# Optimization experiments

Measured on AMD Instinct MI355X. Metric: run time of the kernel, lower is better.

Reference implementation:

```python
import jax, jax.numpy as jnp
import numpy as np

N_NODES = 50000
N_EDGES = 800000
C_FEAT = 96
HID = 96
C_CONST = 0.005


def _psi(v):
    return jnp.sign(v) * jnp.log(jnp.abs(v) + 1.0)


def setup_inputs() -> dict:
    key = jax.random.key(0)
    ks = jax.random.split(key, 16)
    d_e_in = 2 * C_FEAT + 2
    d_h_in = 2 * C_FEAT
    def w(k, fan_in, fan_out):
        return jax.random.normal(k, (fan_in, fan_out), jnp.float32) * (1.0 / np.sqrt(fan_in))
    return {
        "x": jax.random.normal(ks[0], (N_NODES, 4), jnp.float32),
        "h": jax.random.normal(ks[1], (N_NODES, C_FEAT), jnp.float32),
        "edge_i": jax.random.randint(ks[2], (N_EDGES,), 0, N_NODES, jnp.int32),
        "edge_j": jax.random.randint(ks[3], (N_EDGES,), 0, N_NODES, jnp.int32),
        "We1": w(ks[4], d_e_in, HID), "be1": jnp.zeros((HID,), jnp.float32),
        "We2": w(ks[5], HID, HID), "be2": jnp.zeros((HID,), jnp.float32),
        "Wm": w(ks[6], HID, 1), "bm": jnp.zeros((1,), jnp.float32),
        "Wh1": w(ks[7], d_h_in, HID), "bh1": jnp.zeros((HID,), jnp.float32),
        "Wh2": w(ks[8], HID, C_FEAT), "bh2": jnp.zeros((C_FEAT,), jnp.float32),
        "Wx1": w(ks[9], HID, HID), "bx1": jnp.zeros((HID,), jnp.float32),
        "Wx2": w(ks[10], HID, 1),  # bias-free last phi_x layer
    }


def reference(x, h, edge_i, edge_j, We1, be1, We2, be2, Wm, bm,
              Wh1, bh1, Wh2, bh2, Wx1, bx1, Wx2):
    n = x.shape[0]
    x_i = x[edge_i]            # (K,4)
    x_j = x[edge_j]            # (K,4)
    # Minkowski invariants: 2*t-component - full Euclidean sum == (+,-,-,-)
    d2 = jnp.square(x_i - x_j)
    norms = 2.0 * d2[..., 0] - jnp.sum(d2, axis=-1)
    z = x_i * x_j
    prods = 2.0 * z[..., 0] - jnp.sum(z, axis=-1)
    norms = _psi(norms)[:, None]   # (K,1)
    prods = _psi(prods)[:, None]   # (K,1)

    e_in = jnp.concatenate([h[edge_i], h[edge_j], norms, prods], axis=-1)  # (K,2C+2)
    m = jax.nn.relu(jax.nn.relu(e_in @ We1 + be1) @ We2 + be2)             # (K,HID)
    w_gate = jax.nn.sigmoid(m @ Wm + bm)                                   # (K,1)

    wm = jax.ops.segment_sum(w_gate * m, edge_i, num_segments=n)          # (N,HID)
    dh = jax.nn.relu(jnp.concatenate([h, wm], axis=-1) @ Wh1 + bh1) @ Wh2 + bh2
    h_out = h + dh

    phi_x = jax.nn.relu(m @ Wx1 + bx1) @ Wx2                              # (K,1)
    vals = phi_x * x_j                                                     # (K,4)
    s = jax.ops.segment_sum(vals, edge_i, num_segments=n)                 # (N,4)
    cnt = jax.ops.segment_sum(jnp.ones((vals.shape[0],), vals.dtype), edge_i, num_segments=n)
    mean = jnp.where(cnt[:, None] > 0, s / jnp.maximum(cnt[:, None], 1.0), 0.0)
    x_out = x + C_CONST * mean
    return (h_out, x_out)
```

## Files before the change

### kernel.cpp

```cpp
#include <hip/hip_runtime.h>
#include <math.h>

#define NN 50000
#define NE 800000
#define NB 196
#define TE 128

typedef __attribute__((ext_vector_type(8))) _Float16 half8v;
typedef __attribute__((ext_vector_type(2))) _Float16 half2v;
typedef __attribute__((ext_vector_type(4))) float f32x4;

__device__ __forceinline__ unsigned short f2h_us(float f) {
  const _Float16 h = (_Float16)f;
  return *(const unsigned short*)&h;
}
__device__ __forceinline__ unsigned pk2h(float a, float b) {
  half2v h; h[0] = (_Float16)a; h[1] = (_Float16)b;
  return *(unsigned*)&h;
}

__global__ void kprep(const int* __restrict__ ei, int* __restrict__ cnt,
                      const float* __restrict__ We1, const float* __restrict__ We2,
                      const float* __restrict__ Wx1, const float* __restrict__ Wh1,
                      const float* __restrict__ Wh2,
                      unsigned short* __restrict__ We1p, unsigned short* __restrict__ We2p,
                      unsigned short* __restrict__ Wx1p, unsigned short* __restrict__ Wh1p,
                      unsigned short* __restrict__ Wh2p, unsigned* __restrict__ WA2,
                      unsigned* __restrict__ WB2) {
  const int b = blockIdx.x;
  if (b < NE / 256) {
    const int i = b * 256 + threadIdx.x;
    atomicAdd(&cnt[ei[i]], 1);
    return;
  }
  const int t = (b - NE / 256) * 256 + threadIdx.x;
  const int j = t & 7, lane = (t >> 3) & 63;
  const int kk = (lane >> 4) * 8 + j;
  const int nn = lane & 15;
  {
    const int tile = t >> 9, tk = tile / 12, tn = tile % 12;
    const int k = tk * 32 + kk, n2 = tn * 16 + nn;
    const float v = (n2 < 96) ? We1[k * 96 + n2] : We1[(96 + k) * 96 + (n2 - 96)];
    We1p[t] = f2h_us(v);
  }
  {
    const int tile = t >> 9, tk = tile / 6, tn = tile % 6;
    const int k = tk * 32 + kk, n = tn * 16 + nn;
    Wh1p[t] = f2h_us(Wh1[k * 96 + n]);
  }
  if (t < 9216) {
    const int tile = t >> 9, tk = tile / 6, tn = tile % 6;
    const int k = tk * 32 + kk, n = tn * 16 + nn;
    We2p[t] = f2h_us(We2[k * 96 + n]);
    Wx1p[t] = f2h_us(Wx1[k * 96 + n]);
    Wh2p[t] = f2h_us(Wh2[k * 96 + n]);
  }
  if (t < 48) {
    WA2[t] = pk2h(We1[192 * 96 + 2 * t], We1[192 * 96 + 2 * t + 1]);
    WB2[t] = pk2h(We1[193 * 96 + 2 * t], We1[193 * 96 + 2 * t + 1]);
  }
}

__global__ void kscanA(const int* __restrict__ cnt, int* __restrict__ pre,
                       int* __restrict__ bsum) {
  __shared__ int ps[256];
  const int b = blockIdx.x, t = threadIdx.x, idx = b * 256 + t;
  const int v = (idx < NN) ? cnt[idx] : 0;
  ps[t] = v;
  __syncthreads();
  for (int off = 1; off < 256; off <<= 1) {
    const int u = (t >= off) ? ps[t - off] : 0;
    __syncthreads();
    ps[t] += u;
    __syncthreads();
  }
  if (idx < NN) pre[idx] = ps[t] - v;
  if (t == 255) bsum[b] = ps[255];
}

__global__ void kscanBC(const int* __restrict__ pre, const int* __restrict__ bsum,
                        int* __restrict__ base, int* __restrict__ cursor) {
  __shared__ int ws[4];
  const int b = blockIdx.x, t = threadIdx.x;
  int s = (t < b) ? bsum[t] : 0;
  s += __shfl_xor(s, 1);  s += __shfl_xor(s, 2);  s += __shfl_xor(s, 4);
  s += __shfl_xor(s, 8);  s += __shfl_xor(s, 16); s += __shfl_xor(s, 32);
  if ((t & 63) == 0) ws[t >> 6] = s;
  __syncthreads();
  const int boff = ws[0] + ws[1] + ws[2] + ws[3];
  const int idx = b * 256 + t;
  if (idx < NN) {
    const int v = pre[idx] + boff;
    base[idx] = v;
    cursor[idx] = v;
  }
  if (idx == 0) base[NN] = NE;
}

__global__ void kperm(const int* __restrict__ ei, const int* __restrict__ ej,
                      int* __restrict__ cursor, int2* __restrict__ ep,
                      float* __restrict__ wz) {
  const int i = blockIdx.x * 256 + threadIdx.x;
  if (i < 625000) {
    const float4 z = make_float4(0.f, 0.f, 0.f, 0.f);
    *(float4*)(wz + (size_t)i * 8) = z;
    *(float4*)(wz + (size_t)i * 8 + 4) = z;
  }
  const int vi = ei[i];
  const int pos = atomicAdd(&cursor[vi], 1);
  ep[pos] = make_int2(vi, ej[i]);
}

__global__ __launch_bounds__(256, 4) void k0_AB(const float* __restrict__ h,
                                                const unsigned short* __restrict__ We1p,
                                                const float* __restrict__ be1,
                                                unsigned short* __restrict__ Ahf,
                                                unsigned short* __restrict__ Bhf) {
  __shared__ __align__(16) unsigned short hbT[64 * 104];
  __shared__ __align__(16) unsigned short outT[64 * 200];
  const int tid = threadIdx.x;
  const int nb = blockIdx.x * 64;
  {
    const int e = tid & 63, q = tid >> 6;
    const int node = nb + e;
    const int nc = node < NN ? node : NN - 1;
    const float* hr = h + (long)nc * 96 + q * 24;
    unsigned* dst = (unsigned*)hbT + e * 52 + q * 12;
    #pragma unroll
    for (int c = 0; c < 6; ++c) {
      const float4 v = *(const float4*)(hr + c * 4);
      dst[c * 2]     = pk2h(v.x, v.y);
      dst[c * 2 + 1] = pk2h(v.z, v.w);
    }
  }
  __syncthreads();
  const int l = tid & 63, w = tid >> 6, cg = l & 15, rg = l >> 4;
  {
    const half8v* Wp = (const half8v*)We1p;
    const unsigned short* ar = hbT + (w * 16 + cg) * 104;
    const half8v af0 = *(const half8v*)(ar + rg * 8);
    const half8v af1 = *(const half8v*)(ar + 32 + rg * 8);
    const half8v af2 = *(const half8v*)(ar + 64 + rg * 8);
    #pragma unroll
    for (int tn = 0; tn < 12; ++tn) {
      f32x4 acc = (f32x4){0.f, 0.f, 0.f, 0.f};
      acc = __builtin_amdgcn_mfma_f32_16x16x32_f16(af0, Wp[(0 * 12 + tn) * 64 + l], acc, 0, 0, 0);
      acc = __builtin_amdgcn_mfma_f32_16x16x32_f16(af1, Wp[(1 * 12 + tn) * 64 + l], acc, 0, 0, 0);
      acc = __builtin_amdgcn_mfma_f32_16x16x32_f16(af2, Wp[(2 * 12 + tn) * 64 + l], acc, 0, 0, 0);
      const float bb = (tn < 6) ? be1[tn * 16 + cg] : 0.f;
      #pragma unroll
      for (int r = 0; r < 4; ++r)
        outT[(w * 16 + rg * 4 + r) * 200 + tn * 16 + cg] = f2h_us(acc[r] + bb);
    }
  }
  __syncthreads();
  {
    const int e = tid & 63, q = tid >> 6;
    const int node = nb + e;
    if (node < NN) {
      const unsigned* src = (const unsigned*)outT + e * 100;
      if (q < 2) {
        uint4* dA = (uint4*)(Ahf + (size_t)node * 96);
        #pragma unroll
        for (int i = 0; i < 6; ++i) dA[q * 6 + i] = *(const uint4*)(src + (q * 6 + i) * 4);
      } else {
        uint4* dB = (uint4*)(Bhf + (size_t)node * 96);
        #pragma unroll
        for (int i = 0; i < 6; ++i) dB[(q - 2) * 6 + i] = *(const uint4*)(src + 48 + ((q - 2) * 6 + i) * 4);
      }
    }
  }
}

__global__ __launch_bounds__(256, 5) void k1_edge(const float* __restrict__ x,
    const unsigned short* __restrict__ Ahf, const unsigned short* __restrict__ Bhf,
    const int2* __restrict__ ep,
    const unsigned* __restrict__ WA2, const unsigned* __restrict__ WB2,
    const unsigned short* __restrict__ We2p, const float* __restrict__ be2,
    const float* __restrict__ Wm, const float* __restrict__ bm,
    const unsigned short* __restrict__ Wx1p, const float* __restrict__ bx1,
    const float* __restrict__ Wx2,
    float* __restrict__ wmo, float* __restrict__ svo) {
  __shared__ __align__(16) unsigned short actT[TE * 104];
  __shared__ float gl[TE];
  __shared__ float phil[TE];
  __shared__ __align__(16) float xjl[TE * 4];
  __shared__ int vseq[TE + 2];
  __shared__ unsigned long long bmask[2];

  const int tid = threadIdx.x;
  const float bm0 = bm[0];
  const int tb = blockIdx.x * TE;

  {
    const int e2 = tid & 127, hf = tid >> 7;
    const int fb = hf * 48;
    const int2 v2 = ep[tb + e2];
    const int vi = v2.x, vj = v2.y;
    const float4 xi = *(const float4*)(x + (long)vi * 4);
    const float4 xj = *(const float4*)(x + (long)vj * 4);
    if (hf == 0) {
      vseq[1 + e2] = vi;
      *(float4*)(xjl + e2 * 4) = xj;
    }
    if (tid == 0) {
      vseq[0] = (tb > 0) ? ep[tb - 1].x : -1;
      vseq[TE + 1] = (tb + TE < NE) ? ep[tb + TE].x : -1;
    }
    const float d0 = xi.x - xj.x, d1 = xi.y - xj.y, d2 = xi.z - xj.z, d3 = xi.w - xj.w;
    const float nrm = d0 * d0 - d1 * d1 - d2 * d2 - d3 * d3;
    const float prd = xi.x * xj.x - xi.y * xj.y - xi.z * xj.z - xi.w * xj.w;
    const float pn = copysignf(logf(fabsf(nrm) + 1.f), nrm);
    const float pp = copysignf(logf(fabsf(prd) + 1.f), prd);
    half2v pn2; pn2[0] = (_Float16)pn; pn2[1] = (_Float16)pn;
    half2v pp2; pp2[0] = (_Float16)pp; pp2[1] = (_Float16)pp;
    const half2v z2 = (half2v){(_Float16)0.f, (_Float16)0.f};
    const uint4* Ar = (const uint4*)(Ahf + (size_t)vi * 96 + fb);
    const uint4* Br = (const uint4*)(Bhf + (size_t)vj * 96 + fb);
    const half2v* wa2 = (const half2v*)(WA2 + fb / 2);
    const half2v* wb2 = (const half2v*)(WB2 + fb / 2);
    unsigned* arow = (unsigned*)actT + e2 * 52 + hf * 24;
    #pragma unroll
    for (int c = 0; c < 6; ++c) {
      const uint4 A4 = Ar[c], B4 = Br[c];
      const half2v* a2 = (const half2v*)&A4;
      const half2v* b2 = (const half2v*)&B4;
      #pragma unroll
      for (int k2 = 0; k2 < 4; ++k2) {
        half2v t = a2[k2] + b2[k2];
        t = pn2 * wa2[c * 4 + k2] + t;
        t = pp2 * wb2[c * 4 + k2] + t;
        t = __builtin_elementwise_max(t, z2);
        arow[c * 4 + k2] = *(unsigned*)&t;
      }
    }
  }
  __syncthreads();

  if (tid < TE) {
    const int pred = (vseq[1 + tid] != vseq[2 + tid]) ? 1 : 0;
    const unsigned long long mk = __ballot(pred);
    if ((tid & 63) == 0) bmask[tid >> 6] = mk;
  }

  const int l = tid & 63, w = tid >> 6;
  const int cg = l & 15, rg = l >> 4;
  const int r0 = w * 32;
  const half8v* Wp2 = (const half8v*)We2p;
  const half8v* Wpx = (const half8v*)Wx1p;

  {
    half8v af[2][3];
    #pragma unroll
    for (int rt = 0; rt < 2; ++rt)
      #pragma unroll
      for (int tk = 0; tk < 3; ++tk)
        af[rt][tk] = *(const half8v*)(actT + (r0 + rt * 16 + cg) * 104 + tk * 32 + rg * 8);
    f32x4 acc[2][6];
    #pragma unroll
    for (int rt = 0; rt < 2; ++rt)
      #pragma unroll
      for (int tn = 0; tn < 6; ++tn) acc[rt][tn] = (f32x4){0.f, 0.f, 0.f, 0.f};
    #pragma unroll
    for (int tk = 0; tk < 3; ++tk)
      #pragma unroll
      for (int tn = 0; tn < 6; ++tn) {
        const half8v bf = Wp2[(tk * 6 + tn) * 64 + l];
        acc[0][tn] = __builtin_amdgcn_mfma_f32_16x16x32_f16(af[0][tk], bf, acc[0][tn], 0, 0, 0);
        acc[1][tn] = __builtin_amdgcn_mfma_f32_16x16x32_f16(af[1][tk], bf, acc[1][tn], 0, 0, 0);
      }
    #pragma unroll
    for (int rt = 0; rt < 2; ++rt) {
      float gp[4] = {0.f, 0.f, 0.f, 0.f};
      #pragma unroll
      for (int tn = 0; tn < 6; ++tn) {
        const int col = tn * 16 + cg;
        const float b = be2[col], wmw = Wm[col];
        #pragma unroll
        for (int r = 0; r < 4; ++r) {
          const float v = fmaxf(acc[rt][tn][r] + b, 0.f);
          gp[r] = fmaf(v, wmw, gp[r]);
          actT[(r0 + rt * 16 + rg * 4 + r) * 104 + col] = f2h_us(v);
        }
      }
      #pragma unroll
      for (int r = 0; r < 4; ++r) {
        float s = gp[r];
        s += __shfl_xor(s, 1); s += __shfl_xor(s, 2);
        s += __shfl_xor(s, 4); s += __shfl_xor(s, 8);
        if (cg == 0) gl[r0 + rt * 16 + rg * 4 + r] = 1.f / (1.f + expf(-(s + bm0)));
      }
    }
  }


  {
    half8v af[2][3];
    #pragma unroll
    for (int rt = 0; rt < 2; ++rt)
      #pragma unroll
      for (int tk = 0; tk < 3; ++tk)
        af[rt][tk] = *(const half8v*)(actT + (r0 + rt * 16 + cg) * 104 + tk * 32 + rg * 8);
    f32x4 acc[2][6];
    #pragma unroll
    for (int rt = 0; rt < 2; ++rt)
      #pragma unroll
      for (int tn = 0; tn < 6; ++tn) acc[rt][tn] = (f32x4){0.f, 0.f, 0.f, 0.f};
    #pragma unroll
    for (int tk = 0; tk < 3; ++tk)
      #pragma unroll
      for (int tn = 0; tn < 6; ++tn) {
        const half8v bf = Wpx[(tk * 6 + tn) * 64 + l];
        acc[0][tn] = __builtin_amdgcn_mfma_f32_16x16x32_f16(af[0][tk], bf, acc[0][tn], 0, 0, 0);
        acc[1][tn] = __builtin_amdgcn_mfma_f32_16x16x32_f16(af[1][tk], bf, acc[1][tn], 0, 0, 0);
      }
    #pragma unroll
    for (int rt = 0; rt < 2; ++rt) {
      float pp2[4] = {0.f, 0.f, 0.f, 0.f};
      #pragma unroll
      for (int tn = 0; tn < 6; ++tn) {
        const int col = tn * 16 + cg;
        const float b = bx1[col], wxw = Wx2[col];
        #pragma unroll
        for (int r = 0; r < 4; ++r)
          pp2[r] = fmaf(fmaxf(acc[rt][tn][r] + b, 0.f), wxw, pp2[r]);
      }
      #pragma unroll
      for (int r = 0; r < 4; ++r) {
        float s = pp2[r];
        s += __shfl_xor(s, 1); s += __shfl_xor(s, 2);
        s += __shfl_xor(s, 4); s += __shfl_xor(s, 8);
        if (cg == 0) phil[r0 + rt * 16 + rg * 4 + r] = s;
      }
    }
  }
  __syncthreads();

  if (tid < 192) {
    const int p = tid % 48;
    const int q = tid / 48;
    const int s_lo = q * 32;
    const unsigned long long mk = bmask[s_lo >> 6];
    float a0 = 0.f, a1 = 0.f;
    bool clean = (q == 0) ? (vseq[0] != vseq[1])
                          : (((bmask[(s_lo - 1) >> 6] >> ((s_lo - 1) & 63)) & 1ull) != 0);
    for (int i = 0; i < 32; ++i) {
      const int e = s_lo + i;
      const half2v h2 = *(const half2v*)(actT + e * 104 + 2 * p);
      const float g = gl[e];
      a0 = fmaf(g, (float)h2[0], a0);
      a1 = fmaf(g, (float)h2[1], a1);
      const bool gend = ((mk >> (e & 63)) & 1ull) != 0;
      if (gend || i == 31) {
        const int node = vseq[e + 1];
        float* dst = wmo + (size_t)node * 96 + 2 * p;
        if (clean && gend) {
          *(float2*)dst = make_float2(a0, a1);
        } else {
          atomicAdd(dst, a0);
          atomicAdd(dst + 1, a1);
        }
        a0 = a1 = 0.f; clean = true;
      }
    }
  } else if (tid < 224) {
    const int t2 = tid - 192;
    const int comp = t2 & 3, q8 = t2 >> 2;
    const int s_lo = q8 * 16;
    const unsigned long long mk = bmask[s_lo >> 6];
    float acc2 = 0.f;
    bool clean = (q8 == 0) ? (vseq[0] != vseq[1])
                           : (((bmask[(s_lo - 1) >> 6] >> ((s_lo - 1) & 63)) & 1ull) != 0);
    for (int i = 0; i < 16; ++i) {
      const int e = s_lo + i;
      acc2 = fmaf(phil[e], xjl[e * 4 + comp], acc2);
      const bool gend = ((mk >> (e & 63)) & 1ull) != 0;
      if (gend || i == 15) {
        const int node = vseq[e + 1];
        float* dst = svo + (size_t)node * 4 + comp;
        if (clean && gend) *dst = acc2; else atomicAdd(dst, acc2);
        acc2 = 0.f; clean = true;
      }
    }
  }
}

__global__ __launch_bounds__(256, 4) void k3ab(const float* __restrict__ h,
    const float* __restrict__ wmv,
    const unsigned short* __restrict__ Wh1p, const float* __restrict__ bh1,
    const unsigned short* __restrict__ Wh2p, const float* __restrict__ bh2,
    const float* __restrict__ x, const float* __restrict__ svm,
    const int* __restrict__ basep,
    float* __restrict__ hout, float* __restrict__ xout) {
  __shared__ __align__(16) unsigned short inT[64 * 200];
  __shared__ __align__(16) unsigned short tmpT[64 * 104];
  const int tid = threadIdx.x;
  const int nb = blockIdx.x * 64;
  const int l = tid & 63, w = tid >> 6, cg = l & 15, rg = l >> 4;
  {
    const int r = w * 16 + (l & 15);
    const int cg2 = l >> 4;
    const int node = nb + r;
    const int nc = node < NN ? node : NN - 1;
    const float* hr = h + (long)nc * 96 + cg2 * 24;
    const float* wr = wmv + (long)nc * 96 + cg2 * 24;
    unsigned* dh = (unsigned*)inT + r * 100 + cg2 * 12;
    unsigned* dw = (unsigned*)inT + r * 100 + 48 + cg2 * 12;
    #pragma unroll
    for (int c = 0; c < 6; ++c) {
      const float4 v = *(const float4*)(hr + c * 4);
      dh[c * 2]     = pk2h(v.x, v.y);
      dh[c * 2 + 1] = pk2h(v.z, v.w);
      const float4 u = *(const float4*)(wr + c * 4);
      dw[c * 2]     = pk2h(u.x, u.y);
      dw[c * 2 + 1] = pk2h(u.z, u.w);
    }
  }
  {
    const unsigned short* ar = inT + (w * 16 + cg) * 200;
    half8v af[6];
    #pragma unroll
    for (int tk = 0; tk < 6; ++tk) af[tk] = *(const half8v*)(ar + tk * 32 + rg * 8);
    const half8v* Wp = (const half8v*)Wh1p;
    #pragma unroll
    for (int tn = 0; tn < 6; ++tn) {
      f32x4 acc = (f32x4){0.f, 0.f, 0.f, 0.f};
      #pragma unroll
      for (int tk = 0; tk < 6; ++tk)
        acc = __builtin_amdgcn_mfma_f32_16x16x32_f16(af[tk], Wp[(tk * 6 + tn) * 64 + l], acc, 0, 0, 0);
      const int col = tn * 16 + cg;
      const float b = bh1[col];
      #pragma unroll
      for (int r = 0; r < 4; ++r)
        tmpT[(w * 16 + rg * 4 + r) * 104 + col] = f2h_us(fmaxf(acc[r] + b, 0.f));
    }
  }
  {
    float* oT = (float*)inT;
    const unsigned short* mr = tmpT + (w * 16 + cg) * 104;
    const half8v mf0 = *(const half8v*)(mr + rg * 8);
    const half8v mf1 = *(const half8v*)(mr + 32 + rg * 8);
    const half8v mf2 = *(const half8v*)(mr + 64 + rg * 8);
    const half8v* Wp = (const half8v*)Wh2p;
    #pragma unroll
    for (int tn = 0; tn < 6; ++tn) {
      f32x4 acc = (f32x4){0.f, 0.f, 0.f, 0.f};
      acc = __builtin_amdgcn_mfma_f32_16x16x32_f16(mf0, Wp[(0 * 6 + tn) * 64 + l], acc, 0, 0, 0);
      acc = __builtin_amdgcn_mfma_f32_16x16x32_f16(mf1, Wp[(1 * 6 + tn) * 64 + l], acc, 0, 0, 0);
      acc = __builtin_amdgcn_mfma_f32_16x16x32_f16(mf2, Wp[(2 * 6 + tn) * 64 + l], acc, 0, 0, 0);
      const int col = tn * 16 + cg;
      const float b = bh2[col];
      #pragma unroll
      for (int r = 0; r < 4; ++r)
        oT[(w * 16 + rg * 4 + r) * 100 + col] = acc[r] + b;
    }
  }
  __syncthreads();
  {
    const int e = tid & 63, q = tid >> 6;
    const int node = nb + e;
    if (node < NN) {
      const float* src = (const float*)inT + e * 100 + q * 24;
      const float* hr = h + (size_t)node * 96 + q * 24;
      float* dst = hout + (size_t)node * 96 + q * 24;
      #pragma unroll
      for (int c = 0; c < 6; ++c) {
        const float4 s = *(const float4*)(src + c * 4);
        const float4 hv = *(const float4*)(hr + c * 4);
        *(float4*)(dst + c * 4) = make_float4(hv.x + s.x, hv.y + s.y, hv.z + s.z, hv.w + s.w);
      }
    }
  }
  if (tid < 64) {
    const int node = nb + tid;
    if (node < NN) {
      const int cnt = basep[node + 1] - basep[node];
      const float inv = cnt > 0 ? 1.f / (float)cnt : 0.f;
      const float4 s4 = *(const float4*)(svm + (long)node * 4);
      const float4 xv = *(const float4*)(x + (long)node * 4);
      *(float4*)(xout + (long)node * 4) =
          make_float4(xv.x + 0.005f * s4.x * inv, xv.y + 0.005f * s4.y * inv,
                      xv.z + 0.005f * s4.z * inv, xv.w + 0.005f * s4.w * inv);
    }
  }
}

extern "C" void kernel_launch(void* const* d_in, const int* in_sizes, int n_in,
                              void* d_out, int out_size, void* d_ws, size_t ws_size,
                              hipStream_t stream) {
  const float* x   = (const float*)d_in[0];
  const float* h   = (const float*)d_in[1];
  const int*   ei  = (const int*)d_in[2];
  const int*   ej  = (const int*)d_in[3];
  const float* We1 = (const float*)d_in[4];
  const float* be1 = (const float*)d_in[5];
  const float* We2 = (const float*)d_in[6];
  const float* be2 = (const float*)d_in[7];
  const float* Wm  = (const float*)d_in[8];
  const float* bm  = (const float*)d_in[9];
  const float* Wh1 = (const float*)d_in[10];
  const float* bh1 = (const float*)d_in[11];
  const float* Wh2 = (const float*)d_in[12];
  const float* bh2 = (const float*)d_in[13];
  const float* Wx1 = (const float*)d_in[14];
  const float* bx1 = (const float*)d_in[15];
  const float* Wx2 = (const float*)d_in[16];

  char* w = (char*)d_ws;
  unsigned short* Ahf  = (unsigned short*)w;
  unsigned short* Bhf  = (unsigned short*)(w + 9600000);
  float* WMv  = (float*)(w + 19200000);
  float* SvM  = (float*)(w + 38400000);
  int*   cnt  = (int*)(w + 39200000);
  int*   base = (int*)(w + 39400000);
  int*   curs = (int*)(w + 39600064);
  unsigned short* We2p = (unsigned short*)(w + 39800064);
  unsigned short* Wx1p = (unsigned short*)(w + 39818496);
  unsigned short* We1p = (unsigned short*)(w + 39836928);
  unsigned short* Wh1p = (unsigned short*)(w + 39873792);
  unsigned short* Wh2p = (unsigned short*)(w + 39910656);
  unsigned* WA2 = (unsigned*)(w + 39929088);
  unsigned* WB2 = (unsigned*)(w + 39929280);
  int2*  epb  = (int2*)(w + 39930112);
  int*   pre  = (int*)(w + 46330112);
  int*   bsum = (int*)(w + 46530112);

  float* hout = (float*)d_out;
  float* xout = hout + 4800000;

  hipMemsetAsync(cnt, 0, NN * sizeof(int), stream);
  kprep<<<NE / 256 + 72, 256, 0, stream>>>(ei, cnt, We1, We2, Wx1, Wh1, Wh2,
                                           We1p, We2p, Wx1p, Wh1p, Wh2p, WA2, WB2);
  kscanA<<<NB, 256, 0, stream>>>(cnt, pre, bsum);
  kscanBC<<<NB, 256, 0, stream>>>(pre, bsum, base, curs);
  kperm<<<NE / 256, 256, 0, stream>>>(ei, ej, curs, epb, WMv);
  k0_AB<<<782, 256, 0, stream>>>(h, We1p, be1, Ahf, Bhf);
  k1_edge<<<NE / TE, 256, 0, stream>>>(x, Ahf, Bhf, epb, WA2, WB2, We2p, be2,
                                       Wm, bm, Wx1p, bx1, Wx2, WMv, SvM);
  k3ab<<<782, 256, 0, stream>>>(h, WMv, Wh1p, bh1, Wh2p, bh2, x, SvM, base, hout, xout);
}
```

Before: 270.5 us.

## Double edge-kernel block size so each wave computes sixteen edge rows

The edge kernel now launches 512 threads per block while still handling 128 edges. The work is redistributed across phases: the first-layer gather uses quarter-row feature slices, each wave runs the MFMA for one 16-row tile instead of two, and the segmented reductions cover 16-edge chunks. The goal is more waves in flight and lower register pressure per thread, to hide gather and MFMA latency. In exchange, each weight fragment is reused across half as many rows, so weight loads per edge double. Shorter reduction chunks also add more chunk boundaries and therefore more atomic adds.

```diff
diff --git a/kernel.cpp b/kernel.cpp
--- a/kernel.cpp
+++ b/kernel.cpp
@@ -172,7 +172,7 @@
   }
 }
 
-__global__ __launch_bounds__(256, 5) void k1_edge(const float* __restrict__ x,
+__global__ __launch_bounds__(512, 6) void k1_edge(const float* __restrict__ x,
     const unsigned short* __restrict__ Ahf, const unsigned short* __restrict__ Bhf,
     const int2* __restrict__ ep,
     const unsigned* __restrict__ WA2, const unsigned* __restrict__ WB2,
@@ -193,13 +193,13 @@
   const int tb = blockIdx.x * TE;
 
   {
-    const int e2 = tid & 127, hf = tid >> 7;
-    const int fb = hf * 48;
+    const int e2 = tid & 127, qf = tid >> 7;
+    const int fb = qf * 24;
     const int2 v2 = ep[tb + e2];
     const int vi = v2.x, vj = v2.y;
     const float4 xi = *(const float4*)(x + (long)vi * 4);
     const float4 xj = *(const float4*)(x + (long)vj * 4);
-    if (hf == 0) {
+    if (qf == 0) {
       vseq[1 + e2] = vi;
       *(float4*)(xjl + e2 * 4) = xj;
     }
@@ -219,9 +219,9 @@
     const uint4* Br = (const uint4*)(Bhf + (size_t)vj * 96 + fb);
     const half2v* wa2 = (const half2v*)(WA2 + fb / 2);
     const half2v* wb2 = (const half2v*)(WB2 + fb / 2);
-    unsigned* arow = (unsigned*)actT + e2 * 52 + hf * 24;
-    #pragma unroll
-    for (int c = 0; c < 6; ++c) {
+    unsigned* arow = (unsigned*)actT + e2 * 52 + qf * 12;
+    #pragma unroll
+    for (int c = 0; c < 3; ++c) {
       const uint4 A4 = Ar[c], B4 = Br[c];
       const half2v* a2 = (const half2v*)&A4;
       const half2v* b2 = (const half2v*)&B4;
@@ -245,113 +245,93 @@
 
   const int l = tid & 63, w = tid >> 6;
   const int cg = l & 15, rg = l >> 4;
-  const int r0 = w * 32;
+  const int r0 = w * 16;
   const half8v* Wp2 = (const half8v*)We2p;
   const half8v* Wpx = (const half8v*)Wx1p;
 
   {
-    half8v af[2][3];
-    #pragma unroll
-    for (int rt = 0; rt < 2; ++rt)
-      #pragma unroll
-      for (int tk = 0; tk < 3; ++tk)
-        af[rt][tk] = *(const half8v*)(actT + (r0 + rt * 16 + cg) * 104 + tk * 32 + rg * 8);
-    f32x4 acc[2][6];
-    #pragma unroll
-    for (int rt = 0; rt < 2; ++rt)
-      #pragma unroll
-      for (int tn = 0; tn < 6; ++tn) acc[rt][tn] = (f32x4){0.f, 0.f, 0.f, 0.f};
+    half8v af[3];
     #pragma unroll
     for (int tk = 0; tk < 3; ++tk)
-      #pragma unroll
-      for (int tn = 0; tn < 6; ++tn) {
-        const half8v bf = Wp2[(tk * 6 + tn) * 64 + l];
-        acc[0][tn] = __builtin_amdgcn_mfma_f32_16x16x32_f16(af[0][tk], bf, acc[0][tn], 0, 0, 0);
-        acc[1][tn] = __builtin_amdgcn_mfma_f32_16x16x32_f16(af[1][tk], bf, acc[1][tn], 0, 0, 0);
+      af[tk] = *(const half8v*)(actT + (r0 + cg) * 104 + tk * 32 + rg * 8);
+    f32x4 acc[6];
+    #pragma unroll
+    for (int tn = 0; tn < 6; ++tn) acc[tn] = (f32x4){0.f, 0.f, 0.f, 0.f};
+    #pragma unroll
+    for (int tk = 0; tk < 3; ++tk)
+      #pragma unroll
+      for (int tn = 0; tn < 6; ++tn)
+        acc[tn] = __builtin_amdgcn_mfma_f32_16x16x32_f16(af[tk], Wp2[(tk * 6 + tn) * 64 + l], acc[tn], 0, 0, 0);
+    float gp[4] = {0.f, 0.f, 0.f, 0.f};
+    #pragma unroll
+    for (int tn = 0; tn < 6; ++tn) {
+      const int col = tn * 16 + cg;
+      const float b = be2[col], wmw = Wm[col];
+      #pragma unroll
+      for (int r = 0; r < 4; ++r) {
+        const float v = fmaxf(acc[tn][r] + b, 0.f);
+        gp[r] = fmaf(v, wmw, gp[r]);
+        actT[(r0 + rg * 4 + r) * 104 + col] = f2h_us(v);
       }
-    #pragma unroll
-    for (int rt = 0; rt < 2; ++rt) {
-      float gp[4] = {0.f, 0.f, 0.f, 0.f};
-      #pragma unroll
-      for (int tn = 0; tn < 6; ++tn) {
-        const int col = tn * 16 + cg;
-        const float b = be2[col], wmw = Wm[col];
-        #pragma unroll
-        for (int r = 0; r < 4; ++r) {
-          const float v = fmaxf(acc[rt][tn][r] + b, 0.f);
-          gp[r] = fmaf(v, wmw, gp[r]);
-          actT[(r0 + rt * 16 + rg * 4 + r) * 104 + col] = f2h_us(v);
-        }
-      }
-      #pragma unroll
-      for (int r = 0; r < 4; ++r) {
-        float s = gp[r];
-        s += __shfl_xor(s, 1); s += __shfl_xor(s, 2);
-        s += __shfl_xor(s, 4); s += __shfl_xor(s, 8);
-        if (cg == 0) gl[r0 + rt * 16 + rg * 4 + r] = 1.f / (1.f + expf(-(s + bm0)));
-      }
-    }
-  }
-
-
-  {
-    half8v af[2][3];
-    #pragma unroll
-    for (int rt = 0; rt < 2; ++rt)
-      #pragma unroll
-      for (int tk = 0; tk < 3; ++tk)
-        af[rt][tk] = *(const half8v*)(actT + (r0 + rt * 16 + cg) * 104 + tk * 32 + rg * 8);
-    f32x4 acc[2][6];
-    #pragma unroll
-    for (int rt = 0; rt < 2; ++rt)
-      #pragma unroll
-      for (int tn = 0; tn < 6; ++tn) acc[rt][tn] = (f32x4){0.f, 0.f, 0.f, 0.f};
+    }
+    #pragma unroll
+    for (int r = 0; r < 4; ++r) {
+      float s = gp[r];
+      s += __shfl_xor(s, 1); s += __shfl_xor(s, 2);
+      s += __shfl_xor(s, 4); s += __shfl_xor(s, 8);
+      if (cg == 0) gl[r0 + rg * 4 + r] = 1.f / (1.f + expf(-(s + bm0)));
+    }
+  }
+
+
+  {
+    half8v af[3];
     #pragma unroll
     for (int tk = 0; tk < 3; ++tk)
-      #pragma unroll
-      for (int tn = 0; tn < 6; ++tn) {
-        const half8v bf = Wpx[(tk * 6 + tn) * 64 + l];
-        acc[0][tn] = __builtin_amdgcn_mfma_f32_16x16x32_f16(af[0][tk], bf, acc[0][tn], 0, 0, 0);
-        acc[1][tn] = __builtin_amdgcn_mfma_f32_16x16x32_f16(af[1][tk], bf, acc[1][tn], 0, 0, 0);
-      }
-    #pragma unroll
-    for (int rt = 0; rt < 2; ++rt) {
-      float pp2[4] = {0.f, 0.f, 0.f, 0.f};
-      #pragma unroll
-      for (int tn = 0; tn < 6; ++tn) {
-        const int col = tn * 16 + cg;
-        const float b = bx1[col], wxw = Wx2[col];
-        #pragma unroll
-        for (int r = 0; r < 4; ++r)
-          pp2[r] = fmaf(fmaxf(acc[rt][tn][r] + b, 0.f), wxw, pp2[r]);
-      }
-      #pragma unroll
-      for (int r = 0; r < 4; ++r) {
-        float s = pp2[r];
-        s += __shfl_xor(s, 1); s += __shfl_xor(s, 2);
-        s += __shfl_xor(s, 4); s += __shfl_xor(s, 8);
-        if (cg == 0) phil[r0 + rt * 16 + rg * 4 + r] = s;
-      }
-    }
-  }
-  __syncthreads();
-
-  if (tid < 192) {
+      af[tk] = *(const half8v*)(actT + (r0 + cg) * 104 + tk * 32 + rg * 8);
+    f32x4 acc[6];
+    #pragma unroll
+    for (int tn = 0; tn < 6; ++tn) acc[tn] = (f32x4){0.f, 0.f, 0.f, 0.f};
+    #pragma unroll
+    for (int tk = 0; tk < 3; ++tk)
+      #pragma unroll
+      for (int tn = 0; tn < 6; ++tn)
+        acc[tn] = __builtin_amdgcn_mfma_f32_16x16x32_f16(af[tk], Wpx[(tk * 6 + tn) * 64 + l], acc[tn], 0, 0, 0);
+    float pq[4] = {0.f, 0.f, 0.f, 0.f};
+    #pragma unroll
+    for (int tn = 0; tn < 6; ++tn) {
+      const int col = tn * 16 + cg;
+      const float b = bx1[col], wxw = Wx2[col];
+      #pragma unroll
+      for (int r = 0; r < 4; ++r)
+        pq[r] = fmaf(fmaxf(acc[tn][r] + b, 0.f), wxw, pq[r]);
+    }
+    #pragma unroll
+    for (int r = 0; r < 4; ++r) {
+      float s = pq[r];
+      s += __shfl_xor(s, 1); s += __shfl_xor(s, 2);
+      s += __shfl_xor(s, 4); s += __shfl_xor(s, 8);
+      if (cg == 0) phil[r0 + rg * 4 + r] = s;
+    }
+  }
+  __syncthreads();
+
+  if (tid < 384) {
     const int p = tid % 48;
-    const int q = tid / 48;
-    const int s_lo = q * 32;
+    const int q8 = tid / 48;
+    const int s_lo = q8 * 16;
     const unsigned long long mk = bmask[s_lo >> 6];
     float a0 = 0.f, a1 = 0.f;
-    bool clean = (q == 0) ? (vseq[0] != vseq[1])
-                          : (((bmask[(s_lo - 1) >> 6] >> ((s_lo - 1) & 63)) & 1ull) != 0);
-    for (int i = 0; i < 32; ++i) {
+    bool clean = (q8 == 0) ? (vseq[0] != vseq[1])
+                           : (((bmask[(s_lo - 1) >> 6] >> ((s_lo - 1) & 63)) & 1ull) != 0);
+    for (int i = 0; i < 16; ++i) {
       const int e = s_lo + i;
       const half2v h2 = *(const half2v*)(actT + e * 104 + 2 * p);
       const float g = gl[e];
       a0 = fmaf(g, (float)h2[0], a0);
       a1 = fmaf(g, (float)h2[1], a1);
       const bool gend = ((mk >> (e & 63)) & 1ull) != 0;
-      if (gend || i == 31) {
+      if (gend || i == 15) {
         const int node = vseq[e + 1];
         float* dst = wmo + (size_t)node * 96 + 2 * p;
         if (clean && gend) {
@@ -363,8 +343,8 @@
         a0 = a1 = 0.f; clean = true;
       }
     }
-  } else if (tid < 224) {
-    const int t2 = tid - 192;
+  } else if (tid < 416) {
+    const int t2 = tid - 384;
     const int comp = t2 & 3, q8 = t2 >> 2;
     const int s_lo = q8 * 16;
     const unsigned long long mk = bmask[s_lo >> 6];
@@ -535,7 +515,7 @@
   kscanBC<<<NB, 256, 0, stream>>>(pre, bsum, base, curs);
   kperm<<<NE / 256, 256, 0, stream>>>(ei, ej, curs, epb, WMv);
   k0_AB<<<782, 256, 0, stream>>>(h, We1p, be1, Ahf, Bhf);
-  k1_edge<<<NE / TE, 256, 0, stream>>>(x, Ahf, Bhf, epb, WA2, WB2, We2p, be2,
+  k1_edge<<<NE / TE, 512, 0, stream>>>(x, Ahf, Bhf, epb, WA2, WB2, We2p, be2,
                                        Wm, bm, Wx1p, bx1, Wx2, WMv, SvM);
   k3ab<<<782, 256, 0, stream>>>(h, WMv, Wh1p, bh1, Wh2p, bh2, x, SvM, base, hout, xout);
 }
```

Measured after the change: 260.3 us. 3.8% less time.
